# Performance work log

Hardware: AMD Instinct MI355X
Metric: run time of the kernel (lower is better)

The kernel has to match this reference:

```python
import jax, jax.numpy as jnp
import numpy as np

ALPHA = 0.2  # LeakyReLU negative slope
EPS = 1e-16


def setup_inputs() -> dict:
    key = jax.random.key(0)
    k0, k1, k2, k3 = jax.random.split(key, 4)
    N, E, F_in, F_out, HEADS = 50000, 1600000, 256, 128, 4
    H = jax.random.normal(k0, (N, F_in), dtype=jnp.float32)
    edge_index = jax.random.randint(k1, (2, E), 0, N)  # row0=src, row1=dst
    # Xavier-ish scaled params
    W = jax.random.normal(k2, (HEADS, F_out, F_in), dtype=jnp.float32) * (1.0 / np.sqrt(F_in))
    a = jax.random.normal(k3, (HEADS, 2 * F_out), dtype=jnp.float32) * 0.1
    bias = jnp.zeros((F_out,), dtype=jnp.float32)
    return {"H": H, "edge_index": edge_index, "W": W, "a": a, "bias": bias}


def reference(H, edge_index, W, a, bias):
    """GAT layer: per-head edge attention + segment softmax over src + SpMM, mean over heads.

    H: [N, F_in]; edge_index: [2, E]; W: [heads, F_out, F_in]; a: [heads, 2*F_out]; bias: [F_out]
    Note: a(concat(h_src, h_dst)) == h_src @ a[:F_out] + h_dst @ a[F_out:], so we compute the
    two per-node scores once on nodes instead of materializing the E x 2*F_out concat.
    """
    N = H.shape[0]
    heads, F_out, _ = W.shape
    src, dst = edge_index[0], edge_index[1]
    outs = []
    for h in range(heads):
        Ht = H @ W[h].T                      # [N, F_out]
        s_src = Ht @ a[h, :F_out]            # [N]
        s_dst = Ht @ a[h, F_out:]            # [N]
        e = s_src[src] + s_dst[dst]          # [E]
        e = jnp.where(e > 0, e, ALPHA * e)   # LeakyReLU
        # segment softmax over src nodes (matches scatter amax + scatter_add)
        e_max = jax.ops.segment_max(e, src, num_segments=N)    # [N], -inf for isolated nodes
        e_exp = jnp.exp(e - e_max[src])                         # [E]
        denom = jax.ops.segment_sum(e_exp, src, num_segments=N) # [N]
        attn = e_exp / (denom[src] + EPS)                       # [E]
        # sparse.mm(attention, Ht): out[i] = sum_{(i,j) in E} attn_ij * Ht[j]
        out = jax.ops.segment_sum(attn[:, None] * Ht[dst], src, num_segments=N)  # [N, F_out]
        outs.append(out)
    final = jnp.mean(jnp.stack(outs, axis=0), axis=0) + bias
    return final
```

## Files before the change

kernel.cpp:

```cpp
#include <hip/hip_runtime.h>

#define ALPHA 0.2f
#define EPS 1e-16f

static constexpr int F_IN = 256;
static constexpr int F_OUT = 128;
static constexpr int HEADS = 4;
static constexpr int COLS = HEADS * F_OUT;
static constexpr int NCH = 64;

typedef __bf16 bf16x8 __attribute__((ext_vector_type(8)));
typedef float f32x4 __attribute__((ext_vector_type(4)));

static __device__ __forceinline__ unsigned short f2bf(float f) {
  unsigned int u = __float_as_uint(f);
  unsigned int r = (u + 0x7FFFu + ((u >> 16) & 1u)) >> 16;
  return (unsigned short)r;
}
static __device__ __forceinline__ float bf_lo(unsigned int u) {
  return __uint_as_float(u << 16);
}
static __device__ __forceinline__ float bf_hi(unsigned int u) {
  return __uint_as_float(u & 0xFFFF0000u);
}
static __device__ __forceinline__ void cvt8(const float4& p0, const float4& p1, bf16x8& v) {
  v[0] = (__bf16)p0.x; v[1] = (__bf16)p0.y; v[2] = (__bf16)p0.z; v[3] = (__bf16)p0.w;
  v[4] = (__bf16)p1.x; v[5] = (__bf16)p1.y; v[6] = (__bf16)p1.z; v[7] = (__bf16)p1.w;
}

__global__ __launch_bounds__(256) void k_merged(int mode, int Cb, int start, int len,
    const float* __restrict__ A, const float* __restrict__ Wf,
    unsigned char* __restrict__ Hq, unsigned char* __restrict__ rec,
    float* __restrict__ ssrc, const float* __restrict__ Av, int N,
    const int* __restrict__ src, unsigned short* __restrict__ bcnt,
    int* __restrict__ cnt, int* __restrict__ bsum, int* __restrict__ off,
    unsigned int* __restrict__ base32, int E, int RNG, int Npad, int nscan) {
  __shared__ union {
    unsigned int bins[6272];
    struct { __bf16 As[128][40]; __bf16 Bs[128][40]; float sS[128]; float sD[128]; } g;
    int ws[4];
    int sbuf[256];
  } u;
  const int t = threadIdx.x;

  if ((int)blockIdx.x >= Cb) {
    const int j = (int)blockIdx.x - Cb;
    const int q8 = len >> 3, r8 = len & 7;
    const int x = j & 7, ii = j >> 3;
    const int p = start + ((x < r8) ? x * (q8 + 1) + ii
                                    : r8 * (q8 + 1) + (x - r8) * q8 + ii);
    const int by = p >> 2;
    const int bx = p & 3;
    const int w = t >> 6, l = t & 63;
    const int wr = w >> 1, wc = w & 1;
    const int m0 = by << 7, n0 = bx << 7;
    const int lr = t >> 1, seg16 = (t & 1) << 4;
    int ar = m0 + lr; if (ar >= N) ar = N - 1;
    const float* Ap = A + (size_t)ar * F_IN + seg16;
    const float* Wp = Wf + (size_t)(n0 + lr) * F_IN + seg16;
    f32x4 acc[4][4] = {};
    for (int k0 = 0; k0 < F_IN; k0 += 32) {
      const float4 f0 = *(const float4*)(Ap + k0);
      const float4 f1 = *(const float4*)(Ap + k0 + 4);
      const float4 f2 = *(const float4*)(Ap + k0 + 8);
      const float4 f3 = *(const float4*)(Ap + k0 + 12);
      const float4 g0 = *(const float4*)(Wp + k0);
      const float4 g1 = *(const float4*)(Wp + k0 + 4);
      const float4 g2 = *(const float4*)(Wp + k0 + 8);
      const float4 g3 = *(const float4*)(Wp + k0 + 12);
      bf16x8 v0, v1, u0, u1;
      cvt8(f0, f1, v0); cvt8(f2, f3, v1);
      cvt8(g0, g1, u0); cvt8(g2, g3, u1);
      __syncthreads();
      *(bf16x8*)&u.g.As[lr][seg16] = v0;  *(bf16x8*)&u.g.As[lr][seg16 + 8] = v1;
      *(bf16x8*)&u.g.Bs[lr][seg16] = u0;  *(bf16x8*)&u.g.Bs[lr][seg16 + 8] = u1;
      __syncthreads();
      const int kb = (l >> 4) << 3;
      bf16x8 af[4], bf_[4];
#pragma unroll
      for (int mi = 0; mi < 4; ++mi)
        af[mi] = *(const bf16x8*)&u.g.As[(wr << 6) + (mi << 4) + (l & 15)][kb];
#pragma unroll
      for (int ni = 0; ni < 4; ++ni)
        bf_[ni] = *(const bf16x8*)&u.g.Bs[(wc << 6) + (ni << 4) + (l & 15)][kb];
#pragma unroll
      for (int mi = 0; mi < 4; ++mi)
#pragma unroll
        for (int ni = 0; ni < 4; ++ni)
          acc[mi][ni] = __builtin_amdgcn_mfma_f32_16x16x32_bf16(af[mi], bf_[ni], acc[mi][ni], 0, 0, 0);
    }
    {
      float as_[4], ad_[4];
#pragma unroll
      for (int ni = 0; ni < 4; ++ni) {
        const int f = (wc << 6) + (ni << 4) + (l & 15);
        as_[ni] = Av[bx * 256 + f];
        ad_[ni] = Av[bx * 256 + 128 + f];
      }
#pragma unroll
      for (int mi = 0; mi < 4; ++mi)
#pragma unroll
        for (int r = 0; r < 4; ++r) {
          float ds_ = 0.f, dd_ = 0.f;
#pragma unroll
          for (int ni = 0; ni < 4; ++ni) {
            ds_ = fmaf(acc[mi][ni][r], as_[ni], ds_);
            dd_ = fmaf(acc[mi][ni][r], ad_[ni], dd_);
          }
#pragma unroll
          for (int m = 1; m < 16; m <<= 1) {
            ds_ += __shfl_xor(ds_, m);
            dd_ += __shfl_xor(dd_, m);
          }
          if (wc == 0 && (l & 15) == 0) {
            const int rl = (wr << 6) + (mi << 4) + ((l >> 4) << 2) + r;
            u.g.sS[rl] = ds_; u.g.sD[rl] = dd_;
          }
        }
      __syncthreads();
      if (wc == 1) {
#pragma unroll
        for (int mi = 0; mi < 4; ++mi)
#pragma unroll
          for (int r = 0; r < 4; ++r) {
            float ds_ = 0.f, dd_ = 0.f;
#pragma unroll
            for (int ni = 0; ni < 4; ++ni) {
              ds_ = fmaf(acc[mi][ni][r], as_[ni], ds_);
              dd_ = fmaf(acc[mi][ni][r], ad_[ni], dd_);
            }
#pragma unroll
            for (int m = 1; m < 16; m <<= 1) {
              ds_ += __shfl_xor(ds_, m);
              dd_ += __shfl_xor(dd_, m);
            }
            if ((l & 15) == 0) {
              const int rl = (wr << 6) + (mi << 4) + ((l >> 4) << 2) + r;
              const int row = m0 + rl;
              if (row < N) {
                ssrc[row * 4 + bx] = u.g.sS[rl] + ds_;
                *(float*)&rec[(size_t)row * 32 + (bx << 2)] = u.g.sD[rl] + dd_;
              }
            }
          }
      }
    }
    const int bxg = (bx << 1) + wc;
#pragma unroll
    for (int mi = 0; mi < 4; ++mi)
#pragma unroll
      for (int r = 0; r < 4; ++r) {
        float mx = 0.f;
#pragma unroll
        for (int ni = 0; ni < 4; ++ni) mx = fmaxf(mx, fabsf(acc[mi][ni][r]));
#pragma unroll
        for (int m = 1; m < 16; m <<= 1) mx = fmaxf(mx, __shfl_xor(mx, m));
        const int row = m0 + (wr << 6) + (mi << 4) + ((l >> 4) << 2) + r;
        if (row < N) {
          const float inv = (mx > 0.f) ? 127.f / mx : 0.f;
          if ((l & 15) == 0)
            *(unsigned short*)&rec[(size_t)row * 32 + 16 + (bxg << 1)] = f2bf(mx * (1.f / 127.f));
          unsigned int pk = 0;
#pragma unroll
          for (int ni = 0; ni < 4; ++ni) {
            float tq = fminf(fmaxf(rintf(acc[mi][ni][r] * inv), -127.f), 127.f);
            pk |= ((unsigned int)(((int)tq + 128) & 255)) << (8 * ni);
          }
          *(unsigned int*)&Hq[(size_t)row * 512 + (bxg << 6) + ((l & 15) << 2)] = pk;
        }
      }
    return;
  }

  if (mode == 0) {
    const int ec = blockIdx.x & (NCH - 1), rq = blockIdx.x >> 6;
    const int r0 = rq * RNG;
    const int nw = RNG >> 1;
    for (int jj = t; jj < nw; jj += 256) u.bins[jj] = 0u;
    __syncthreads();
    const int CE = (E + NCH - 1) / NCH;
    const int i0 = ec * CE, i1 = min(E, i0 + CE);
    for (int i = i0 + t; i < i1; i += 256) {
      const unsigned us = (unsigned)(src[i] - r0);
      if (us < (unsigned)RNG) atomicAdd(&u.bins[us >> 1], 1u << ((us & 1) << 4));
    }
    __syncthreads();
    uint4* dv = (uint4*)(bcnt + (size_t)ec * Npad + r0);
    const uint4* sv = (const uint4*)u.bins;
    const int nv = RNG >> 3;
    for (int m = t; m < nv; m += 256) dv[m] = sv[m];
  } else if (mode == 1) {
    const int g = blockIdx.x * 256 + t;
    const int lane = t & 63, w = t >> 6;
    int v = 0;
    if (g < N) {
#pragma unroll 8
      for (int b = 0; b < NCH; ++b) v += bcnt[(size_t)b * Npad + g];
    }
#pragma unroll
    for (int o = 1; o < 64; o <<= 1) {
      const int y = __shfl_up(v, o);
      if (lane >= o) v += y;
    }
    if (lane == 63) u.ws[w] = v;
    __syncthreads();
    if (t == 0) {
      int s = 0;
#pragma unroll
      for (int k = 0; k < 4; ++k) { s += u.ws[k]; u.ws[k] = s; }
    }
    __syncthreads();
    v += (w > 0) ? u.ws[w - 1] : 0;
    if (g < N) cnt[g] = v;
    if (t == 255) bsum[blockIdx.x] = v;
  } else if (mode == 2) {
    if (t < 64) {
      int carry = 0;
      for (int base = 0; base < nscan; base += 64) {
        int v = (base + t < nscan) ? bsum[base + t] : 0;
#pragma unroll
        for (int o = 1; o < 64; o <<= 1) {
          const int y = __shfl_up(v, o);
          if (t >= o) v += y;
        }
        v += carry;
        if (base + t < nscan) u.sbuf[base + t] = v;
        carry = __shfl(v, 63);
      }
    }
    __syncthreads();
    const int g = blockIdx.x * 256 + t;
    if (g == 0) off[0] = 0;
    if (g < N) off[g + 1] = cnt[g] + (blockIdx.x ? u.sbuf[blockIdx.x - 1] : 0);
  } else {
    const int s = blockIdx.x * 256 + t;
    if (s < N) {
      unsigned int run = (unsigned int)off[s];
#pragma unroll 8
      for (int b = 0; b < NCH; ++b) {
        const size_t idx = (size_t)b * Npad + s;
        const unsigned int v = bcnt[idx];
        base32[idx] = run;
        run += v;
      }
    }
  }
}

__global__ __launch_bounds__(256) void k_place(const int* __restrict__ src,
                                               const int* __restrict__ dst,
                                               const unsigned int* __restrict__ base32,
                                               unsigned short* __restrict__ csr,
                                               int E, int RNG, int Npad) {
  __shared__ unsigned int bins[6272];
  const int ec = blockIdx.x & (NCH - 1), rq = blockIdx.x >> 6;
  const int r0 = rq * RNG, t = threadIdx.x;
  const int nw = RNG >> 1;
  for (int jj = t; jj < nw; jj += 256) bins[jj] = 0u;
  __syncthreads();
  const unsigned int* brow = base32 + (size_t)ec * Npad;
  const int CE = (E + NCH - 1) / NCH;
  const int i0 = ec * CE, i1 = min(E, i0 + CE);
  for (int i = i0 + t; i < i1; i += 256) {
    const int s = src[i];
    const unsigned us = (unsigned)(s - r0);
    if (us < (unsigned)RNG) {
      const unsigned int old = atomicAdd(&bins[us >> 1], 1u << ((us & 1) << 4));
      const int local = (old >> ((us & 1) << 4)) & 0xffff;
      csr[brow[s] + local] = (unsigned short)dst[i];
    }
  }
}

__global__ __launch_bounds__(256) void k_spmm(const uint2* __restrict__ Hq2,
    const float4* __restrict__ ssrc4, const unsigned char* __restrict__ rec,
    const int* __restrict__ off, const unsigned short* __restrict__ csr_dst,
    const float* __restrict__ bias, float* __restrict__ out, int N) {
  __shared__ float wbuf[4][8][72];
  __shared__ int   ibuf[4][64];
  const int wv = threadIdx.x >> 6;
  const int lane = threadIdx.x & 63;
  const int n = (blockIdx.x << 2) + wv;
  if (n >= N) return;
  const int hg = lane >> 4;
  const int b8 = lane >> 3;
  const float4 ss4 = ssrc4[n];
  float den4[4] = {};
  float acc[8] = {};
  float sw = 0.f;
  const int beg = off[n], end = off[n + 1];
  for (int c0 = beg; c0 < end; c0 += 64) {
    const int cnt = min(64, end - c0);
    if (lane < cnt) {
      const int d = csr_dst[c0 + lane];
      ibuf[wv][lane] = d << 6;
      const float4 sd4 = *(const float4*)&rec[(size_t)d * 32];
      const uint4  sc  = *(const uint4*)&rec[(size_t)d * 32 + 16];
      float e0 = ss4.x + sd4.x; e0 = fmaxf(e0, ALPHA * e0);
      float e1 = ss4.y + sd4.y; e1 = fmaxf(e1, ALPHA * e1);
      float e2 = ss4.z + sd4.z; e2 = fmaxf(e2, ALPHA * e2);
      float e3 = ss4.w + sd4.w; e3 = fmaxf(e3, ALPHA * e3);
      const float w0 = __expf(e0), w1 = __expf(e1), w2 = __expf(e2), w3 = __expf(e3);
      den4[0] += w0; den4[1] += w1; den4[2] += w2; den4[3] += w3;
      wbuf[wv][0][lane] = w0 * bf_lo(sc.x); wbuf[wv][1][lane] = w0 * bf_hi(sc.x);
      wbuf[wv][2][lane] = w1 * bf_lo(sc.y); wbuf[wv][3][lane] = w1 * bf_hi(sc.y);
      wbuf[wv][4][lane] = w2 * bf_lo(sc.z); wbuf[wv][5][lane] = w2 * bf_hi(sc.z);
      wbuf[wv][6][lane] = w3 * bf_lo(sc.w); wbuf[wv][7][lane] = w3 * bf_hi(sc.w);
    }
#pragma unroll 8
    for (int j = 0; j < cnt; ++j) {
      const float wgt = wbuf[wv][b8][j];
      const int db = ibuf[wv][j];
      const uint2 q = Hq2[db + lane];
      sw += wgt;
      acc[0] = fmaf(wgt, (float)(q.x & 0xffu),         acc[0]);
      acc[1] = fmaf(wgt, (float)((q.x >> 8) & 0xffu),  acc[1]);
      acc[2] = fmaf(wgt, (float)((q.x >> 16) & 0xffu), acc[2]);
      acc[3] = fmaf(wgt, (float)(q.x >> 24),           acc[3]);
      acc[4] = fmaf(wgt, (float)(q.y & 0xffu),         acc[4]);
      acc[5] = fmaf(wgt, (float)((q.y >> 8) & 0xffu),  acc[5]);
      acc[6] = fmaf(wgt, (float)((q.y >> 16) & 0xffu), acc[6]);
      acc[7] = fmaf(wgt, (float)(q.y >> 24),           acc[7]);
    }
  }
#pragma unroll
  for (int k = 0; k < 4; ++k)
#pragma unroll
    for (int m = 1; m < 64; m <<= 1) den4[k] += __shfl_xor(den4[k], m);
  const float r = 1.f / (den4[hg] + EPS);
  const float corr = 128.f * sw;
#pragma unroll
  for (int i = 0; i < 8; ++i) acc[i] = (acc[i] - corr) * r;
#pragma unroll
  for (int i = 0; i < 8; ++i) {
    acc[i] += __shfl_xor(acc[i], 16);
    acc[i] += __shfl_xor(acc[i], 32);
  }
  if (lane < 16) {
    const int base = ((lane >> 3) & 1) * 64 + ((lane & 7) << 1);
#pragma unroll
    for (int k = 0; k < 4; ++k) {
      const float2 b2 = *(const float2*)&bias[base + k * 16];
      *(float2*)&out[(size_t)n * F_OUT + base + k * 16] =
          make_float2(0.25f * acc[k] + b2.x, 0.25f * acc[k + 4] + b2.y);
    }
  }
}

extern "C" void kernel_launch(void* const* d_in, const int* in_sizes, int n_in,
                              void* d_out, int out_size, void* d_ws, size_t ws_size,
                              hipStream_t stream) {
  const float* H    = (const float*)d_in[0];
  const int*   ei   = (const int*)d_in[1];
  const float* W    = (const float*)d_in[2];
  const float* a    = (const float*)d_in[3];
  const float* bias = (const float*)d_in[4];
  const int N = in_sizes[0] / F_IN;
  const int E = in_sizes[1] / 2;
  const int* src = ei;
  const int* dst = ei + E;

  const int RNG  = ((((N + 3) >> 2) + 7) & ~7);
  const int Npad = RNG * 4;
  const int nscan = (N + 255) / 256;

  char* ws = (char*)d_ws;
  size_t o = 0;
  auto alloc = [&](size_t bytes) -> void* {
    void* p = ws + o;
    o = (o + bytes + 255) & ~(size_t)255;
    return p;
  };
  unsigned char*  Hq  = (unsigned char*)alloc((size_t)N * COLS);
  float* ssrc = (float*)alloc((size_t)N * HEADS * sizeof(float));
  unsigned char* rec = (unsigned char*)alloc((size_t)N * 32);
  int*   cnt  = (int*)alloc((size_t)N * sizeof(int));
  int*   off  = (int*)alloc(((size_t)N + 1) * sizeof(int));
  unsigned short* csr  = (unsigned short*)alloc((size_t)E * sizeof(unsigned short));
  unsigned short* bcnt = (unsigned short*)alloc((size_t)NCH * Npad * 2);
  unsigned int*  base  = (unsigned int*)alloc((size_t)NCH * Npad * 4);
  int*   bsum = (int*)alloc((size_t)nscan * sizeof(int));

  const int Tg = 4 * ((N + 127) / 128);
  const int c0 = (Tg + 3) / 4;
  const int starts[4] = {0, c0, 2 * c0, 3 * c0};
  const int lens[4]   = {c0, c0, c0, Tg - 3 * c0};

  k_merged<<<256 + lens[0], 256, 0, stream>>>(0, 256, starts[0], lens[0],
      H, W, Hq, rec, ssrc, a, N, src, bcnt, cnt, bsum, off, base, E, RNG, Npad, nscan);
  k_merged<<<nscan + lens[1], 256, 0, stream>>>(1, nscan, starts[1], lens[1],
      H, W, Hq, rec, ssrc, a, N, src, bcnt, cnt, bsum, off, base, E, RNG, Npad, nscan);
  k_merged<<<nscan + lens[2], 256, 0, stream>>>(2, nscan, starts[2], lens[2],
      H, W, Hq, rec, ssrc, a, N, src, bcnt, cnt, bsum, off, base, E, RNG, Npad, nscan);
  k_merged<<<nscan + lens[3], 256, 0, stream>>>(3, nscan, starts[3], lens[3],
      H, W, Hq, rec, ssrc, a, N, src, bcnt, cnt, bsum, off, base, E, RNG, Npad, nscan);

  k_place<<<256, 256, 0, stream>>>(src, dst, base, csr, E, RNG, Npad);
  k_spmm<<<(N + 3) / 4, 256, 0, stream>>>((const uint2*)Hq, (const float4*)ssrc,
                                          rec, off, csr, bias, (float*)d_out, N);
}
```

Baseline: 323.2 us.

## Run whole GEMM in one launch with histogram, move scan stages to separate kernels

Previously the GEMM tiles were split across four launches, each co-scheduled with one stage of the CSR build (histogram, column-sum scan, block scan, base computation) to overlap the two. Now all GEMM tiles run in one launch alongside only the histogram, and the three scan stages become small standalone kernels that run afterwards. This gives up overlap of the scan stages with GEMM work, but removes the mode-dispatch overhead and the partial-GEMM tail effects in each launch.

```diff
diff --git a/kernel.cpp b/kernel.cpp
--- a/kernel.cpp
+++ b/kernel.cpp
@@ -28,151 +28,19 @@
   v[4] = (__bf16)p1.x; v[5] = (__bf16)p1.y; v[6] = (__bf16)p1.z; v[7] = (__bf16)p1.w;
 }
 
-__global__ __launch_bounds__(256) void k_merged(int mode, int Cb, int start, int len,
+__global__ __launch_bounds__(256) void k_merged(
     const float* __restrict__ A, const float* __restrict__ Wf,
     unsigned char* __restrict__ Hq, unsigned char* __restrict__ rec,
-    float* __restrict__ ssrc, const float* __restrict__ Av, int N,
+    float* __restrict__ ssrc, const float* __restrict__ Av, int N, int Tg,
     const int* __restrict__ src, unsigned short* __restrict__ bcnt,
-    int* __restrict__ cnt, int* __restrict__ bsum, int* __restrict__ off,
-    unsigned int* __restrict__ base32, int E, int RNG, int Npad, int nscan) {
+    int E, int RNG, int Npad) {
   __shared__ union {
     unsigned int bins[6272];
     struct { __bf16 As[128][40]; __bf16 Bs[128][40]; float sS[128]; float sD[128]; } g;
-    int ws[4];
-    int sbuf[256];
   } u;
   const int t = threadIdx.x;
 
-  if ((int)blockIdx.x >= Cb) {
-    const int j = (int)blockIdx.x - Cb;
-    const int q8 = len >> 3, r8 = len & 7;
-    const int x = j & 7, ii = j >> 3;
-    const int p = start + ((x < r8) ? x * (q8 + 1) + ii
-                                    : r8 * (q8 + 1) + (x - r8) * q8 + ii);
-    const int by = p >> 2;
-    const int bx = p & 3;
-    const int w = t >> 6, l = t & 63;
-    const int wr = w >> 1, wc = w & 1;
-    const int m0 = by << 7, n0 = bx << 7;
-    const int lr = t >> 1, seg16 = (t & 1) << 4;
-    int ar = m0 + lr; if (ar >= N) ar = N - 1;
-    const float* Ap = A + (size_t)ar * F_IN + seg16;
-    const float* Wp = Wf + (size_t)(n0 + lr) * F_IN + seg16;
-    f32x4 acc[4][4] = {};
-    for (int k0 = 0; k0 < F_IN; k0 += 32) {
-      const float4 f0 = *(const float4*)(Ap + k0);
-      const float4 f1 = *(const float4*)(Ap + k0 + 4);
-      const float4 f2 = *(const float4*)(Ap + k0 + 8);
-      const float4 f3 = *(const float4*)(Ap + k0 + 12);
-      const float4 g0 = *(const float4*)(Wp + k0);
-      const float4 g1 = *(const float4*)(Wp + k0 + 4);
-      const float4 g2 = *(const float4*)(Wp + k0 + 8);
-      const float4 g3 = *(const float4*)(Wp + k0 + 12);
-      bf16x8 v0, v1, u0, u1;
-      cvt8(f0, f1, v0); cvt8(f2, f3, v1);
-      cvt8(g0, g1, u0); cvt8(g2, g3, u1);
-      __syncthreads();
-      *(bf16x8*)&u.g.As[lr][seg16] = v0;  *(bf16x8*)&u.g.As[lr][seg16 + 8] = v1;
-      *(bf16x8*)&u.g.Bs[lr][seg16] = u0;  *(bf16x8*)&u.g.Bs[lr][seg16 + 8] = u1;
-      __syncthreads();
-      const int kb = (l >> 4) << 3;
-      bf16x8 af[4], bf_[4];
-#pragma unroll
-      for (int mi = 0; mi < 4; ++mi)
-        af[mi] = *(const bf16x8*)&u.g.As[(wr << 6) + (mi << 4) + (l & 15)][kb];
-#pragma unroll
-      for (int ni = 0; ni < 4; ++ni)
-        bf_[ni] = *(const bf16x8*)&u.g.Bs[(wc << 6) + (ni << 4) + (l & 15)][kb];
-#pragma unroll
-      for (int mi = 0; mi < 4; ++mi)
-#pragma unroll
-        for (int ni = 0; ni < 4; ++ni)
-          acc[mi][ni] = __builtin_amdgcn_mfma_f32_16x16x32_bf16(af[mi], bf_[ni], acc[mi][ni], 0, 0, 0);
-    }
-    {
-      float as_[4], ad_[4];
-#pragma unroll
-      for (int ni = 0; ni < 4; ++ni) {
-        const int f = (wc << 6) + (ni << 4) + (l & 15);
-        as_[ni] = Av[bx * 256 + f];
-        ad_[ni] = Av[bx * 256 + 128 + f];
-      }
-#pragma unroll
-      for (int mi = 0; mi < 4; ++mi)
-#pragma unroll
-        for (int r = 0; r < 4; ++r) {
-          float ds_ = 0.f, dd_ = 0.f;
-#pragma unroll
-          for (int ni = 0; ni < 4; ++ni) {
-            ds_ = fmaf(acc[mi][ni][r], as_[ni], ds_);
-            dd_ = fmaf(acc[mi][ni][r], ad_[ni], dd_);
-          }
-#pragma unroll
-          for (int m = 1; m < 16; m <<= 1) {
-            ds_ += __shfl_xor(ds_, m);
-            dd_ += __shfl_xor(dd_, m);
-          }
-          if (wc == 0 && (l & 15) == 0) {
-            const int rl = (wr << 6) + (mi << 4) + ((l >> 4) << 2) + r;
-            u.g.sS[rl] = ds_; u.g.sD[rl] = dd_;
-          }
-        }
-      __syncthreads();
-      if (wc == 1) {
-#pragma unroll
-        for (int mi = 0; mi < 4; ++mi)
-#pragma unroll
-          for (int r = 0; r < 4; ++r) {
-            float ds_ = 0.f, dd_ = 0.f;
-#pragma unroll
-            for (int ni = 0; ni < 4; ++ni) {
-              ds_ = fmaf(acc[mi][ni][r], as_[ni], ds_);
-              dd_ = fmaf(acc[mi][ni][r], ad_[ni], dd_);
-            }
-#pragma unroll
-            for (int m = 1; m < 16; m <<= 1) {
-              ds_ += __shfl_xor(ds_, m);
-              dd_ += __shfl_xor(dd_, m);
-            }
-            if ((l & 15) == 0) {
-              const int rl = (wr << 6) + (mi << 4) + ((l >> 4) << 2) + r;
-              const int row = m0 + rl;
-              if (row < N) {
-                ssrc[row * 4 + bx] = u.g.sS[rl] + ds_;
-                *(float*)&rec[(size_t)row * 32 + (bx << 2)] = u.g.sD[rl] + dd_;
-              }
-            }
-          }
-      }
-    }
-    const int bxg = (bx << 1) + wc;
-#pragma unroll
-    for (int mi = 0; mi < 4; ++mi)
-#pragma unroll
-      for (int r = 0; r < 4; ++r) {
-        float mx = 0.f;
-#pragma unroll
-        for (int ni = 0; ni < 4; ++ni) mx = fmaxf(mx, fabsf(acc[mi][ni][r]));
-#pragma unroll
-        for (int m = 1; m < 16; m <<= 1) mx = fmaxf(mx, __shfl_xor(mx, m));
-        const int row = m0 + (wr << 6) + (mi << 4) + ((l >> 4) << 2) + r;
-        if (row < N) {
-          const float inv = (mx > 0.f) ? 127.f / mx : 0.f;
-          if ((l & 15) == 0)
-            *(unsigned short*)&rec[(size_t)row * 32 + 16 + (bxg << 1)] = f2bf(mx * (1.f / 127.f));
-          unsigned int pk = 0;
-#pragma unroll
-          for (int ni = 0; ni < 4; ++ni) {
-            float tq = fminf(fmaxf(rintf(acc[mi][ni][r] * inv), -127.f), 127.f);
-            pk |= ((unsigned int)(((int)tq + 128) & 255)) << (8 * ni);
-          }
-          *(unsigned int*)&Hq[(size_t)row * 512 + (bxg << 6) + ((l & 15) << 2)] = pk;
-        }
-      }
-    return;
-  }
-
-  if (mode == 0) {
+  if ((int)blockIdx.x < 256) {
     const int ec = blockIdx.x & (NCH - 1), rq = blockIdx.x >> 6;
     const int r0 = rq * RNG;
     const int nw = RNG >> 1;
@@ -189,61 +57,203 @@
     const uint4* sv = (const uint4*)u.bins;
     const int nv = RNG >> 3;
     for (int m = t; m < nv; m += 256) dv[m] = sv[m];
-  } else if (mode == 1) {
-    const int g = blockIdx.x * 256 + t;
-    const int lane = t & 63, w = t >> 6;
-    int v = 0;
-    if (g < N) {
+    return;
+  }
+
+  const int j = (int)blockIdx.x - 256;
+  const int q8 = Tg >> 3, r8 = Tg & 7;
+  const int x = j & 7, ii = j >> 3;
+  const int gp = (x < r8) ? x * (q8 + 1) + ii
+                          : r8 * (q8 + 1) + (x - r8) * q8 + ii;
+  const int by = gp >> 2;
+  const int bx = gp & 3;
+  const int w = t >> 6, l = t & 63;
+  const int wr = w >> 1, wc = w & 1;
+  const int m0 = by << 7, n0 = bx << 7;
+  const int lr = t >> 1, seg16 = (t & 1) << 4;
+  int ar = m0 + lr; if (ar >= N) ar = N - 1;
+  const float* Ap = A + (size_t)ar * F_IN + seg16;
+  const float* Wp = Wf + (size_t)(n0 + lr) * F_IN + seg16;
+  f32x4 acc[4][4] = {};
+  for (int k0 = 0; k0 < F_IN; k0 += 32) {
+    const float4 f0 = *(const float4*)(Ap + k0);
+    const float4 f1 = *(const float4*)(Ap + k0 + 4);
+    const float4 f2 = *(const float4*)(Ap + k0 + 8);
+    const float4 f3 = *(const float4*)(Ap + k0 + 12);
+    const float4 g0 = *(const float4*)(Wp + k0);
+    const float4 g1 = *(const float4*)(Wp + k0 + 4);
+    const float4 g2 = *(const float4*)(Wp + k0 + 8);
+    const float4 g3 = *(const float4*)(Wp + k0 + 12);
+    bf16x8 v0, v1, u0, u1;
+    cvt8(f0, f1, v0); cvt8(f2, f3, v1);
+    cvt8(g0, g1, u0); cvt8(g2, g3, u1);
+    __syncthreads();
+    *(bf16x8*)&u.g.As[lr][seg16] = v0;  *(bf16x8*)&u.g.As[lr][seg16 + 8] = v1;
+    *(bf16x8*)&u.g.Bs[lr][seg16] = u0;  *(bf16x8*)&u.g.Bs[lr][seg16 + 8] = u1;
+    __syncthreads();
+    const int kb = (l >> 4) << 3;
+    bf16x8 af[4], bf_[4];
+#pragma unroll
+    for (int mi = 0; mi < 4; ++mi)
+      af[mi] = *(const bf16x8*)&u.g.As[(wr << 6) + (mi << 4) + (l & 15)][kb];
+#pragma unroll
+    for (int ni = 0; ni < 4; ++ni)
+      bf_[ni] = *(const bf16x8*)&u.g.Bs[(wc << 6) + (ni << 4) + (l & 15)][kb];
+#pragma unroll
+    for (int mi = 0; mi < 4; ++mi)
+#pragma unroll
+      for (int ni = 0; ni < 4; ++ni)
+        acc[mi][ni] = __builtin_amdgcn_mfma_f32_16x16x32_bf16(af[mi], bf_[ni], acc[mi][ni], 0, 0, 0);
+  }
+  {
+    float as_[4], ad_[4];
+#pragma unroll
+    for (int ni = 0; ni < 4; ++ni) {
+      const int f = (wc << 6) + (ni << 4) + (l & 15);
+      as_[ni] = Av[bx * 256 + f];
+      ad_[ni] = Av[bx * 256 + 128 + f];
+    }
+#pragma unroll
+    for (int mi = 0; mi < 4; ++mi)
+#pragma unroll
+      for (int r = 0; r < 4; ++r) {
+        float ds_ = 0.f, dd_ = 0.f;
+#pragma unroll
+        for (int ni = 0; ni < 4; ++ni) {
+          ds_ = fmaf(acc[mi][ni][r], as_[ni], ds_);
+          dd_ = fmaf(acc[mi][ni][r], ad_[ni], dd_);
+        }
+#pragma unroll
+        for (int m = 1; m < 16; m <<= 1) {
+          ds_ += __shfl_xor(ds_, m);
+          dd_ += __shfl_xor(dd_, m);
+        }
+        if (wc == 0 && (l & 15) == 0) {
+          const int rl = (wr << 6) + (mi << 4) + ((l >> 4) << 2) + r;
+          u.g.sS[rl] = ds_; u.g.sD[rl] = dd_;
+        }
+      }
+    __syncthreads();
+    if (wc == 1) {
+#pragma unroll
+      for (int mi = 0; mi < 4; ++mi)
+#pragma unroll
+        for (int r = 0; r < 4; ++r) {
+          float ds_ = 0.f, dd_ = 0.f;
+#pragma unroll
+          for (int ni = 0; ni < 4; ++ni) {
+            ds_ = fmaf(acc[mi][ni][r], as_[ni], ds_);
+            dd_ = fmaf(acc[mi][ni][r], ad_[ni], dd_);
+          }
+#pragma unroll
+          for (int m = 1; m < 16; m <<= 1) {
+            ds_ += __shfl_xor(ds_, m);
+            dd_ += __shfl_xor(dd_, m);
+          }
+          if ((l & 15) == 0) {
+            const int rl = (wr << 6) + (mi << 4) + ((l >> 4) << 2) + r;
+            const int row = m0 + rl;
+            if (row < N) {
+              ssrc[row * 4 + bx] = u.g.sS[rl] + ds_;
+              *(float*)&rec[(size_t)row * 32 + (bx << 2)] = u.g.sD[rl] + dd_;
+            }
+          }
+        }
+    }
+  }
+  const int bxg = (bx << 1) + wc;
+#pragma unroll
+  for (int mi = 0; mi < 4; ++mi)
+#pragma unroll
+    for (int r = 0; r < 4; ++r) {
+      float mx = 0.f;
+#pragma unroll
+      for (int ni = 0; ni < 4; ++ni) mx = fmaxf(mx, fabsf(acc[mi][ni][r]));
+#pragma unroll
+      for (int m = 1; m < 16; m <<= 1) mx = fmaxf(mx, __shfl_xor(mx, m));
+      const int row = m0 + (wr << 6) + (mi << 4) + ((l >> 4) << 2) + r;
+      if (row < N) {
+        const float inv = (mx > 0.f) ? 127.f / mx : 0.f;
+        if ((l & 15) == 0)
+          *(unsigned short*)&rec[(size_t)row * 32 + 16 + (bxg << 1)] = f2bf(mx * (1.f / 127.f));
+        unsigned int pk = 0;
+#pragma unroll
+        for (int ni = 0; ni < 4; ++ni) {
+          float tq = fminf(fmaxf(rintf(acc[mi][ni][r] * inv), -127.f), 127.f);
+          pk |= ((unsigned int)(((int)tq + 128) & 255)) << (8 * ni);
+        }
+        *(unsigned int*)&Hq[(size_t)row * 512 + (bxg << 6) + ((l & 15) << 2)] = pk;
+      }
+    }
+}
+
+__global__ __launch_bounds__(256) void k_colsum_scan1(const unsigned short* __restrict__ bcnt,
+                                                      int* __restrict__ cnt,
+                                                      int* __restrict__ bsum, int N, int Npad) {
+  __shared__ int ws[4];
+  const int t = threadIdx.x, g = blockIdx.x * 256 + t;
+  const int lane = t & 63, w = t >> 6;
+  int v = 0;
+  if (g < N) {
 #pragma unroll 8
-      for (int b = 0; b < NCH; ++b) v += bcnt[(size_t)b * Npad + g];
-    }
-#pragma unroll
-    for (int o = 1; o < 64; o <<= 1) {
-      const int y = __shfl_up(v, o);
-      if (lane >= o) v += y;
-    }
-    if (lane == 63) u.ws[w] = v;
-    __syncthreads();
-    if (t == 0) {
-      int s = 0;
-#pragma unroll
-      for (int k = 0; k < 4; ++k) { s += u.ws[k]; u.ws[k] = s; }
-    }
-    __syncthreads();
-    v += (w > 0) ? u.ws[w - 1] : 0;
-    if (g < N) cnt[g] = v;
-    if (t == 255) bsum[blockIdx.x] = v;
-  } else if (mode == 2) {
-    if (t < 64) {
-      int carry = 0;
-      for (int base = 0; base < nscan; base += 64) {
-        int v = (base + t < nscan) ? bsum[base + t] : 0;
-#pragma unroll
-        for (int o = 1; o < 64; o <<= 1) {
-          const int y = __shfl_up(v, o);
-          if (t >= o) v += y;
-        }
-        v += carry;
-        if (base + t < nscan) u.sbuf[base + t] = v;
-        carry = __shfl(v, 63);
+    for (int b = 0; b < NCH; ++b) v += bcnt[(size_t)b * Npad + g];
+  }
+#pragma unroll
+  for (int o = 1; o < 64; o <<= 1) {
+    const int y = __shfl_up(v, o);
+    if (lane >= o) v += y;
+  }
+  if (lane == 63) ws[w] = v;
+  __syncthreads();
+  if (t == 0) {
+    int s = 0;
+#pragma unroll
+    for (int k = 0; k < 4; ++k) { s += ws[k]; ws[k] = s; }
+  }
+  __syncthreads();
+  v += (w > 0) ? ws[w - 1] : 0;
+  if (g < N) cnt[g] = v;
+  if (t == 255) bsum[blockIdx.x] = v;
+}
+
+__global__ __launch_bounds__(256) void k_scan3(const int* __restrict__ part,
+                                               const int* __restrict__ bsum,
+                                               int* __restrict__ off, int N, int nscan) {
+  __shared__ int sbuf[256];
+  const int t = threadIdx.x;
+  if (t < 64) {
+    int carry = 0;
+    for (int base = 0; base < nscan; base += 64) {
+      int v = (base + t < nscan) ? bsum[base + t] : 0;
+#pragma unroll
+      for (int o = 1; o < 64; o <<= 1) {
+        const int y = __shfl_up(v, o);
+        if (t >= o) v += y;
       }
-    }
-    __syncthreads();
-    const int g = blockIdx.x * 256 + t;
-    if (g == 0) off[0] = 0;
-    if (g < N) off[g + 1] = cnt[g] + (blockIdx.x ? u.sbuf[blockIdx.x - 1] : 0);
-  } else {
-    const int s = blockIdx.x * 256 + t;
-    if (s < N) {
-      unsigned int run = (unsigned int)off[s];
+      v += carry;
+      if (base + t < nscan) sbuf[base + t] = v;
+      carry = __shfl(v, 63);
+    }
+  }
+  __syncthreads();
+  const int g = blockIdx.x * 256 + t;
+  if (g == 0) off[0] = 0;
+  if (g < N) off[g + 1] = part[g] + (blockIdx.x ? sbuf[blockIdx.x - 1] : 0);
+}
+
+__global__ __launch_bounds__(256) void k_base32(const unsigned short* __restrict__ bcnt,
+                                                const int* __restrict__ off,
+                                                unsigned int* __restrict__ base32,
+                                                int N, int Npad) {
+  const int s = blockIdx.x * 256 + threadIdx.x;
+  if (s >= N) return;
+  unsigned int run = (unsigned int)off[s];
 #pragma unroll 8
-      for (int b = 0; b < NCH; ++b) {
-        const size_t idx = (size_t)b * Npad + s;
-        const unsigned int v = bcnt[idx];
-        base32[idx] = run;
-        run += v;
-      }
-    }
+  for (int b = 0; b < NCH; ++b) {
+    const size_t idx = (size_t)b * Npad + s;
+    const unsigned int v = bcnt[idx];
+    base32[idx] = run;
+    run += v;
   }
 }
 
@@ -382,19 +392,12 @@
   int*   bsum = (int*)alloc((size_t)nscan * sizeof(int));
 
   const int Tg = 4 * ((N + 127) / 128);
-  const int c0 = (Tg + 3) / 4;
-  const int starts[4] = {0, c0, 2 * c0, 3 * c0};
-  const int lens[4]   = {c0, c0, c0, Tg - 3 * c0};
-
-  k_merged<<<256 + lens[0], 256, 0, stream>>>(0, 256, starts[0], lens[0],
-      H, W, Hq, rec, ssrc, a, N, src, bcnt, cnt, bsum, off, base, E, RNG, Npad, nscan);
-  k_merged<<<nscan + lens[1], 256, 0, stream>>>(1, nscan, starts[1], lens[1],
-      H, W, Hq, rec, ssrc, a, N, src, bcnt, cnt, bsum, off, base, E, RNG, Npad, nscan);
-  k_merged<<<nscan + lens[2], 256, 0, stream>>>(2, nscan, starts[2], lens[2],
-      H, W, Hq, rec, ssrc, a, N, src, bcnt, cnt, bsum, off, base, E, RNG, Npad, nscan);
-  k_merged<<<nscan + lens[3], 256, 0, stream>>>(3, nscan, starts[3], lens[3],
-      H, W, Hq, rec, ssrc, a, N, src, bcnt, cnt, bsum, off, base, E, RNG, Npad, nscan);
-
+
+  k_merged<<<256 + Tg, 256, 0, stream>>>(H, W, Hq, rec, ssrc, a, N, Tg,
+                                         src, bcnt, E, RNG, Npad);
+  k_colsum_scan1<<<nscan, 256, 0, stream>>>(bcnt, cnt, bsum, N, Npad);
+  k_scan3<<<nscan, 256, 0, stream>>>(cnt, bsum, off, N, nscan);
+  k_base32<<<nscan, 256, 0, stream>>>(bcnt, off, base, N, Npad);
   k_place<<<256, 256, 0, stream>>>(src, dst, base, csr, E, RNG, Npad);
   k_spmm<<<(N + 3) / 4, 256, 0, stream>>>((const uint2*)Hq, (const float4*)ssrc,
                                           rec, off, csr, bias, (float*)d_out, N);
```

Result: faster. 303.5 us (-6.1%).
